# Optimization experiments

Hardware: AMD Instinct MI355X
Metric: run time of the kernel (lower is better)

The kernel has to match this reference:

```python
import jax, jax.numpy as jnp
import numpy as np

B = 131072     # batch of observations
OBS = 17       # HalfCheetah-v5 obs dim
ACT = 6        # HalfCheetah-v5 action dim
M = 16         # number of charts / experts
HID = 256      # encoder / value hidden width (hardcoded in module)
GHID = 128     # gate hidden width (hardcoded)
R = 24.0       # chart radius in whitened feature space
BETA = 1.0     # locality prior strength
NEG = -1e9     # masked-logit fill (finite to keep grads clean)
LOG_STD_MIN, LOG_STD_MAX = -20.0, 2.0


def setup_inputs() -> dict:
    key = jax.random.key(0)
    ks = jax.random.split(key, 12)
    def rn(i, shape, sc):
        return jax.random.normal(ks[i], shape, dtype=jnp.float32) * sc
    return {
        "obs": jax.random.normal(ks[0], (B, OBS), dtype=jnp.float32),
        # encoder MLP (only the two hidden tanh layers feed the feature 'feat')
        "W1": rn(1, (OBS, HID), 0.2), "b1": jnp.zeros((HID,), jnp.float32),
        "W2": rn(2, (HID, HID), 0.06), "b2": jnp.zeros((HID,), jnp.float32),
        # gate: Linear(256,128) -> tanh -> Linear(128,m)
        "Wg1": rn(3, (HID, GHID), 0.06), "bg1": jnp.zeros((GHID,), jnp.float32),
        "Wg2": rn(4, (GHID, M), 0.1), "bg2": jnp.zeros((M,), jnp.float32),
        # m local Gaussian heads: mu Linear(256, act), shared log_std param per head
        "muW": rn(5, (M, HID, ACT), 0.06), "mub": jnp.zeros((M, ACT), jnp.float32),
        "log_std": jnp.zeros((M, ACT), jnp.float32),
        # value head: 256 -> 256 -> 256 -> 1 with tanh
        "Wv1": rn(6, (HID, HID), 0.06), "bv1": jnp.zeros((HID,), jnp.float32),
        "Wv2": rn(7, (HID, HID), 0.06), "bv2": jnp.zeros((HID,), jnp.float32),
        "Wv3": rn(8, (HID, 1), 0.06), "bv3": jnp.zeros((1,), jnp.float32),
        # chart cover state (frozen params in the torch module)
        "centers": jax.random.normal(ks[9], (M, HID), dtype=jnp.float32),
        "stats_mean": jnp.zeros((HID,), jnp.float32),
        "stats_var": jnp.ones((HID,), jnp.float32),
    }


def reference(obs, W1, b1, W2, b2, Wg1, bg1, Wg2, bg2, muW, mub, log_std,
              Wv1, bv1, Wv2, bv2, Wv3, bv3, centers, stats_mean, stats_var):
    # shared encoder phi(o): two tanh layers -> feat [B, HID]
    feat = jnp.tanh(jnp.tanh(obs @ W1 + b1) @ W2 + b2)

    # whitened features and squared distances to chart centers (cdist via gram trick)
    zw = (feat - stats_mean) / jnp.sqrt(stats_var + 1e-6)          # [B, HID]
    d2 = jnp.maximum(
        jnp.sum(zw * zw, axis=-1, keepdims=True)
        + jnp.sum(centers * centers, axis=-1)
        - 2.0 * (zw @ centers.T), 0.0)                              # [B, M]
    dists = jnp.sqrt(d2)

    # gate logits + locality prior -beta * ||z - c_i||^2 / r^2
    logits = jnp.tanh(feat @ Wg1 + bg1) @ Wg2 + bg2 - BETA * d2 / (R * R)

    # masked softmax restricted to active charts; nearest chart always active
    active = dists <= R
    nearest = jax.nn.one_hot(jnp.argmin(dists, axis=1), M, dtype=bool)
    active = active | nearest
    g = jax.nn.softmax(jnp.where(active, logits, NEG), axis=1)      # [B, M]

    # local expert heads mu_i(z), then convex combination of mu and log_std
    mus = jnp.einsum('bd,mda->bma', feat, muW) + mub                # [B, M, ACT]
    mu_bar = jnp.einsum('bm,bma->ba', g, mus)                       # [B, ACT]
    s_bar = jnp.clip(g @ log_std, LOG_STD_MIN, LOG_STD_MAX)         # [B, ACT]

    # value head on shared features
    v = (jnp.tanh(jnp.tanh(feat @ Wv1 + bv1) @ Wv2 + bv2) @ Wv3 + bv3)[:, 0]
    return mu_bar, s_bar, v
```

## Files before the change

### kernel.cpp

```cpp
#include <hip/hip_runtime.h>
#include <hip/hip_bf16.h>

#define BDIM 256
#define TB 64
#define OBS_D 17
#define HID 256
#define GHID 128
#define NM 16
#define NACT 6

typedef __attribute__((ext_vector_type(8))) short short8;
typedef __attribute__((ext_vector_type(4))) float f32x4;

#define OFF_W1P    0u
#define OFF_W2P    16384u
#define OFF_WG1P   147456u
#define OFF_WG2P   212992u
#define OFF_CP     217088u
#define OFF_MUWP   225280u
#define OFF_WV1P   274432u
#define OFF_WV2P   405504u
#define OFF_CNORM  536576u
#define OFF_CCONST 536640u

__device__ __forceinline__ float tanh_fast(float x){
  float e = __expf(2.f * x);
  return fmaf(-2.f, __builtin_amdgcn_rcpf(e + 1.f), 1.f);
}
__device__ __forceinline__ short bf16b(float x){
  __hip_bfloat16 h = __float2bfloat16(x);
  return *reinterpret_cast<short*>(&h);
}

__global__ void prep_kernel(const float* __restrict__ W1, const float* __restrict__ W2,
    const float* __restrict__ Wg1, const float* __restrict__ Wg2,
    const float* __restrict__ muW, const float* __restrict__ Wv1, const float* __restrict__ Wv2,
    const float* __restrict__ centers, const float* __restrict__ smean, const float* __restrict__ svar,
    char* __restrict__ ws)
{
  __hip_bfloat16* w1p  = (__hip_bfloat16*)(ws + OFF_W1P);
  __hip_bfloat16* w2p  = (__hip_bfloat16*)(ws + OFF_W2P);
  __hip_bfloat16* wg1p = (__hip_bfloat16*)(ws + OFF_WG1P);
  __hip_bfloat16* wg2p = (__hip_bfloat16*)(ws + OFF_WG2P);
  __hip_bfloat16* cp   = (__hip_bfloat16*)(ws + OFF_CP);
  __hip_bfloat16* muwp = (__hip_bfloat16*)(ws + OFF_MUWP);
  __hip_bfloat16* wv1p = (__hip_bfloat16*)(ws + OFF_WV1P);
  __hip_bfloat16* wv2p = (__hip_bfloat16*)(ws + OFF_WV2P);
  float* cnorm  = (float*)(ws + OFF_CNORM);
  float* cconst = (float*)(ws + OFF_CCONST);

  int gid = blockIdx.x * blockDim.x + threadIdx.x;
  if (gid < NM){
    float s = 0.f; const float* c = centers + gid * HID;
    for (int k = 0; k < HID; ++k) s += c[k] * c[k];
    cnorm[gid] = s;
  } else if (gid < 2*NM){
    int m = gid - NM; float s = 0.f; const float* c = centers + m * HID;
    for (int k = 0; k < HID; ++k) s += smean[k] * rsqrtf(svar[k] + 1e-6f) * c[k];
    cconst[m] = s;
  }

  const int T0 = 8192, T1 = T0+65536, T2 = T1+32768, T3 = T2+2048,
            T4 = T3+4096, T5 = T4+24576, T6 = T5+65536, T7 = T6+65536;
  for (int i = gid; i < T7; i += gridDim.x * blockDim.x){
    float v; __hip_bfloat16* dst;
    if (i < T0){ int idx=i;    int kb8=idx/(256*8); int n=(idx/8)%256; int e=idx&7; int k=kb8*8+e;
      v = (k < OBS_D) ? W1[k*256+n] : 0.f; dst = &w1p[idx]; }
    else if (i < T1){ int idx=i-T0; int kb8=idx/(256*8); int n=(idx/8)%256; int e=idx&7; int k=kb8*8+e;
      v = W2[k*256+n]; dst = &w2p[idx]; }
    else if (i < T2){ int idx=i-T1; int kb8=idx/(128*8); int n=(idx/8)%128; int e=idx&7; int k=kb8*8+e;
      v = Wg1[k*128+n]; dst = &wg1p[idx]; }
    else if (i < T3){ int idx=i-T2; int kb8=idx/(16*8);  int n=(idx/8)%16;  int e=idx&7; int k=kb8*8+e;
      v = Wg2[k*16+n]; dst = &wg2p[idx]; }
    else if (i < T4){ int idx=i-T3; int kb8=idx/(16*8);  int m=(idx/8)%16;  int e=idx&7; int k=kb8*8+e;
      v = centers[m*HID+k] * rsqrtf(svar[k] + 1e-6f); dst = &cp[idx]; }
    else if (i < T5){ int idx=i-T4; int kb8=idx/(96*8);  int n=(idx/8)%96;  int e=idx&7; int k=kb8*8+e;
      int a = n >> 4, m = n & 15;
      v = muW[m*(HID*NACT) + k*NACT + a]; dst = &muwp[idx]; }
    else if (i < T6){ int idx=i-T5; int kb8=idx/(256*8); int n=(idx/8)%256; int e=idx&7; int k=kb8*8+e;
      v = Wv1[k*256+n]; dst = &wv1p[idx]; }
    else            { int idx=i-T6; int kb8=idx/(256*8); int n=(idx/8)%256; int e=idx&7; int k=kb8*8+e;
      v = Wv2[k*256+n]; dst = &wv2p[idx]; }
    *dst = __float2bfloat16(v);
  }
}

__global__ __launch_bounds__(BDIM, 2) void moe_kernel(
  const float* __restrict__ obs,
  const float* __restrict__ b1, const float* __restrict__ b2,
  const float* __restrict__ bg1, const float* __restrict__ bg2,
  const float* __restrict__ mub, const float* __restrict__ lstd,
  const float* __restrict__ bv1, const float* __restrict__ bv2,
  const float* __restrict__ Wv3, const float* __restrict__ bv3,
  const float* __restrict__ smean, const float* __restrict__ svar,
  const char* __restrict__ ws, float* __restrict__ out, int Btot)
{
  const short8* w1p  = (const short8*)(ws + OFF_W1P);
  const short8* w2p  = (const short8*)(ws + OFF_W2P);
  const short8* wg1p = (const short8*)(ws + OFF_WG1P);
  const short8* wg2p = (const short8*)(ws + OFF_WG2P);
  const short8* cp   = (const short8*)(ws + OFF_CP);
  const short8* muwp = (const short8*)(ws + OFF_MUWP);
  const short8* wv1p = (const short8*)(ws + OFF_WV1P);
  const short8* wv2p = (const short8*)(ws + OFF_WV2P);
  const float* cnorm  = (const float*)(ws + OFF_CNORM);
  const float* cconst = (const float*)(ws + OFF_CCONST);

  const int tid = threadIdx.x;
  const int w = tid >> 6, lane = tid & 63, l16 = lane & 15, lk = lane >> 4;
  const int rowg0 = blockIdx.x * TB;

  __shared__ __hip_bfloat16 feat_s[32*64*8];
  __shared__ __hip_bfloat16 sc_s[32*64*8];
  __shared__ float part_s[4][64];
  __shared__ float g_s[64*17];

  short8 aO[4];
  #pragma unroll
  for (int rt = 0; rt < 4; ++rt){
    const float* orow = obs + (size_t)(rowg0 + rt*16 + l16) * OBS_D;
    #pragma unroll
    for (int e = 0; e < 8; ++e){ int k = lk*8 + e; float v = (k < OBS_D) ? orow[k] : 0.f; aO[rt][e] = bf16b(v); }
  }
  #pragma unroll
  for (int ctl = 0; ctl < 4; ++ctl){
    const int ct = w*4 + ctl;
    short8 B = w1p[lk*256 + ct*16 + l16];
    const int col = ct*16 + l16; const float bb = b1[col];
    #pragma unroll
    for (int rt = 0; rt < 4; ++rt){
      f32x4 acc = {0.f,0.f,0.f,0.f};
      acc = __builtin_amdgcn_mfma_f32_16x16x32_bf16(aO[rt], B, acc, 0,0,0);
      #pragma unroll
      for (int r = 0; r < 4; ++r){
        int row = rt*16 + lk*4 + r;
        sc_s[((col>>3)*64 + row)*8 + (col&7)] = __float2bfloat16(tanh_fast(acc[r] + bb));
      }
    }
  }
  __syncthreads();

  {
    f32x4 acc[4][4];
    #pragma unroll
    for (int i = 0; i < 4; ++i)
      #pragma unroll
      for (int j = 0; j < 4; ++j) acc[i][j] = (f32x4){0.f,0.f,0.f,0.f};
    #pragma unroll
    for (int ck = 0; ck < 8; ++ck){
      short8 A[4];
      #pragma unroll
      for (int rt = 0; rt < 4; ++rt) A[rt] = *(const short8*)&sc_s[((ck*4+lk)*64 + rt*16 + l16)*8];
      #pragma unroll
      for (int ctl = 0; ctl < 4; ++ctl){
        short8 B = w2p[(ck*4+lk)*256 + (w*4+ctl)*16 + l16];
        #pragma unroll
        for (int rt = 0; rt < 4; ++rt)
          acc[ctl][rt] = __builtin_amdgcn_mfma_f32_16x16x32_bf16(A[rt], B, acc[ctl][rt], 0,0,0);
      }
    }
    float znp[16];
    #pragma unroll
    for (int i = 0; i < 16; ++i) znp[i] = 0.f;
    #pragma unroll
    for (int ctl = 0; ctl < 4; ++ctl){
      const int col = (w*4+ctl)*16 + l16;
      const float bb = b2[col], mn = smean[col], iv = rsqrtf(svar[col] + 1e-6f);
      #pragma unroll
      for (int rt = 0; rt < 4; ++rt){
        #pragma unroll
        for (int r = 0; r < 4; ++r){
          int row = rt*16 + lk*4 + r;
          __hip_bfloat16 fb = __float2bfloat16(tanh_fast(acc[ctl][rt][r] + bb));
          feat_s[((col>>3)*64 + row)*8 + (col&7)] = fb;
          float z = (__bfloat162float(fb) - mn) * iv;
          znp[rt*4+r] += z * z;
        }
      }
    }
    #pragma unroll
    for (int d = 1; d < 16; d <<= 1){
      #pragma unroll
      for (int i = 0; i < 16; ++i) znp[i] += __shfl_xor(znp[i], d, 64);
    }
    if (l16 == 0){
      #pragma unroll
      for (int i = 0; i < 16; ++i) part_s[w][(i>>2)*16 + lk*4 + (i&3)] = znp[i];
    }
  }
  __syncthreads();

  {
    f32x4 acc[2][4];
    #pragma unroll
    for (int i = 0; i < 2; ++i)
      #pragma unroll
      for (int j = 0; j < 4; ++j) acc[i][j] = (f32x4){0.f,0.f,0.f,0.f};
    #pragma unroll
    for (int ck = 0; ck < 8; ++ck){
      short8 A[4];
      #pragma unroll
      for (int rt = 0; rt < 4; ++rt) A[rt] = *(const short8*)&feat_s[((ck*4+lk)*64 + rt*16 + l16)*8];
      #pragma unroll
      for (int ctl = 0; ctl < 2; ++ctl){
        short8 B = wg1p[(ck*4+lk)*128 + (w*2+ctl)*16 + l16];
        #pragma unroll
        for (int rt = 0; rt < 4; ++rt)
          acc[ctl][rt] = __builtin_amdgcn_mfma_f32_16x16x32_bf16(A[rt], B, acc[ctl][rt], 0,0,0);
      }
    }
    #pragma unroll
    for (int ctl = 0; ctl < 2; ++ctl){
      const int col = (w*2+ctl)*16 + l16;
      const float bb = bg1[col];
      #pragma unroll
      for (int rt = 0; rt < 4; ++rt)
        #pragma unroll
        for (int r = 0; r < 4; ++r){
          int row = rt*16 + lk*4 + r;
          sc_s[((col>>3)*64 + row)*8 + (col&7)] = __float2bfloat16(tanh_fast(acc[ctl][rt][r] + bb));
        }
    }
  }
  __syncthreads();

  const int rw = w*16;
  short8 fF[8];
  #pragma unroll
  for (int ck = 0; ck < 8; ++ck) fF[ck] = *(const short8*)&feat_s[((ck*4+lk)*64 + rw + l16)*8];

  {
    f32x4 accL = {0.f,0.f,0.f,0.f};
    #pragma unroll
    for (int ks = 0; ks < 4; ++ks){
      short8 aT = *(const short8*)&sc_s[((ks*4+lk)*64 + rw + l16)*8];
      accL = __builtin_amdgcn_mfma_f32_16x16x32_bf16(aT, wg2p[(ks*4+lk)*16 + l16], accL, 0,0,0);
    }
    f32x4 accD = {0.f,0.f,0.f,0.f};
    #pragma unroll
    for (int ck = 0; ck < 8; ++ck)
      accD = __builtin_amdgcn_mfma_f32_16x16x32_bf16(fF[ck], cp[(ck*4+lk)*16 + l16], accD, 0,0,0);

    const float cn = cnorm[l16], cc = cconst[l16], bg2v = bg2[l16];
    float gw[4];
    #pragma unroll
    for (int r = 0; r < 4; ++r){
      int rowl = rw + lk*4 + r;
      float znr = part_s[0][rowl] + part_s[1][rowl] + part_s[2][rowl] + part_s[3][rowl];
      float dot = accD[r] - cc;
      float d2 = fmaxf(znr + cn - 2.f*dot, 0.f);
      float lg = accL[r] + bg2v - d2 * (1.f/(24.f*24.f));
      float mv = d2; int mi = l16;
      #pragma unroll
      for (int d = 1; d < 16; d <<= 1){
        float ov = __shfl_xor(mv, d, 64); int oi = __shfl_xor(mi, d, 64);
        if (ov < mv || (ov == mv && oi < mi)){ mv = ov; mi = oi; }
      }
      bool act = (d2 <= 576.f) || (mi == l16);
      lg = act ? lg : -1e9f;
      float mx = lg;
      #pragma unroll
      for (int d = 1; d < 16; d <<= 1) mx = fmaxf(mx, __shfl_xor(mx, d, 64));
      float ev = __expf(lg - mx);
      float sm = ev;
      #pragma unroll
      for (int d = 1; d < 16; d <<= 1) sm += __shfl_xor(sm, d, 64);
      gw[r] = ev * __builtin_amdgcn_rcpf(sm);
      g_s[rowl*17 + l16] = gw[r];
    }
    #pragma unroll
    for (int r = 0; r < 4; ++r){
      float sb[6];
      #pragma unroll
      for (int a = 0; a < 6; ++a) sb[a] = gw[r] * lstd[l16*6 + a];
      #pragma unroll
      for (int d = 1; d < 16; d <<= 1){
        #pragma unroll
        for (int a = 0; a < 6; ++a) sb[a] += __shfl_xor(sb[a], d, 64);
      }
      if (l16 == 0){
        int row = rowg0 + rw + lk*4 + r;
        #pragma unroll
        for (int a = 0; a < 6; ++a)
          out[(size_t)6*Btot + (size_t)row*6 + a] = fminf(fmaxf(sb[a], -20.f), 2.f);
      }
    }
  }
  __syncthreads();

  {
    const int na = (w < 2) ? 2 : 1;
    const int a0 = (w < 2) ? (w*2) : (w + 2);
    f32x4 acc[2][4];
    #pragma unroll
    for (int i = 0; i < 2; ++i)
      #pragma unroll
      for (int j = 0; j < 4; ++j) acc[i][j] = (f32x4){0.f,0.f,0.f,0.f};
    #pragma unroll
    for (int ck = 0; ck < 8; ++ck){
      short8 A[4];
      #pragma unroll
      for (int rt = 0; rt < 4; ++rt) A[rt] = *(const short8*)&feat_s[((ck*4+lk)*64 + rt*16 + l16)*8];
      #pragma unroll
      for (int al = 0; al < 2; ++al){
        if (al < na){
          short8 B = muwp[(ck*4+lk)*96 + (a0+al)*16 + l16];
          #pragma unroll
          for (int rt = 0; rt < 4; ++rt)
            acc[al][rt] = __builtin_amdgcn_mfma_f32_16x16x32_bf16(A[rt], B, acc[al][rt], 0,0,0);
        }
      }
    }
    #pragma unroll
    for (int al = 0; al < 2; ++al){
      if (al < na){
        const int a = a0 + al;
        const float mubv = mub[l16*6 + a];
        #pragma unroll
        for (int rt = 0; rt < 4; ++rt){
          #pragma unroll
          for (int r = 0; r < 4; ++r){
            int row = rt*16 + lk*4 + r;
            float m = (acc[al][rt][r] + mubv) * g_s[row*17 + l16];
            #pragma unroll
            for (int d = 1; d < 16; d <<= 1) m += __shfl_xor(m, d, 64);
            if (l16 == 0) out[(size_t)(rowg0 + row)*6 + a] = m;
          }
        }
      }
    }
  }

  {
    f32x4 acc[4][4];
    #pragma unroll
    for (int i = 0; i < 4; ++i)
      #pragma unroll
      for (int j = 0; j < 4; ++j) acc[i][j] = (f32x4){0.f,0.f,0.f,0.f};
    #pragma unroll
    for (int ck = 0; ck < 8; ++ck){
      short8 A[4];
      #pragma unroll
      for (int rt = 0; rt < 4; ++rt) A[rt] = *(const short8*)&feat_s[((ck*4+lk)*64 + rt*16 + l16)*8];
      #pragma unroll
      for (int ctl = 0; ctl < 4; ++ctl){
        short8 B = wv1p[(ck*4+lk)*256 + (w*4+ctl)*16 + l16];
        #pragma unroll
        for (int rt = 0; rt < 4; ++rt)
          acc[ctl][rt] = __builtin_amdgcn_mfma_f32_16x16x32_bf16(A[rt], B, acc[ctl][rt], 0,0,0);
      }
    }
    #pragma unroll
    for (int ctl = 0; ctl < 4; ++ctl){
      const int col = (w*4+ctl)*16 + l16;
      const float bb = bv1[col];
      #pragma unroll
      for (int rt = 0; rt < 4; ++rt)
        #pragma unroll
        for (int r = 0; r < 4; ++r){
          int row = rt*16 + lk*4 + r;
          sc_s[((col>>3)*64 + row)*8 + (col&7)] = __float2bfloat16(tanh_fast(acc[ctl][rt][r] + bb));
        }
    }
  }
  __syncthreads();

  {
    f32x4 acc[4][4];
    #pragma unroll
    for (int i = 0; i < 4; ++i)
      #pragma unroll
      for (int j = 0; j < 4; ++j) acc[i][j] = (f32x4){0.f,0.f,0.f,0.f};
    #pragma unroll
    for (int ck = 0; ck < 8; ++ck){
      short8 A[4];
      #pragma unroll
      for (int rt = 0; rt < 4; ++rt) A[rt] = *(const short8*)&sc_s[((ck*4+lk)*64 + rt*16 + l16)*8];
      #pragma unroll
      for (int ctl = 0; ctl < 4; ++ctl){
        short8 B = wv2p[(ck*4+lk)*256 + (w*4+ctl)*16 + l16];
        #pragma unroll
        for (int rt = 0; rt < 4; ++rt)
          acc[ctl][rt] = __builtin_amdgcn_mfma_f32_16x16x32_bf16(A[rt], B, acc[ctl][rt], 0,0,0);
      }
    }
    float vpp[16];
    #pragma unroll
    for (int i = 0; i < 16; ++i) vpp[i] = 0.f;
    #pragma unroll
    for (int ctl = 0; ctl < 4; ++ctl){
      const int col = (w*4+ctl)*16 + l16;
      const float bb = bv2[col], w3 = Wv3[col];
      #pragma unroll
      for (int rt = 0; rt < 4; ++rt)
        #pragma unroll
        for (int r = 0; r < 4; ++r)
          vpp[rt*4+r] += tanh_fast(acc[ctl][rt][r] + bb) * w3;
    }
    #pragma unroll
    for (int d = 1; d < 16; d <<= 1){
      #pragma unroll
      for (int i = 0; i < 16; ++i) vpp[i] += __shfl_xor(vpp[i], d, 64);
    }
    if (l16 == 0){
      #pragma unroll
      for (int i = 0; i < 16; ++i) part_s[w][(i>>2)*16 + lk*4 + (i&3)] = vpp[i];
    }
  }
  __syncthreads();
  if (lane < 16){
    int row = w*16 + lane;
    float v = part_s[0][row] + part_s[1][row] + part_s[2][row] + part_s[3][row] + bv3[0];
    out[(size_t)12*Btot + rowg0 + row] = v;
  }
}

extern "C" void kernel_launch(void* const* d_in, const int* in_sizes, int n_in,
                              void* d_out, int out_size, void* d_ws, size_t ws_size,
                              hipStream_t stream){
  const float* obs = (const float*)d_in[0];
  const float* W1  = (const float*)d_in[1];  const float* b1  = (const float*)d_in[2];
  const float* W2  = (const float*)d_in[3];  const float* b2  = (const float*)d_in[4];
  const float* Wg1 = (const float*)d_in[5];  const float* bg1 = (const float*)d_in[6];
  const float* Wg2 = (const float*)d_in[7];  const float* bg2 = (const float*)d_in[8];
  const float* muW = (const float*)d_in[9];  const float* mub = (const float*)d_in[10];
  const float* lstd= (const float*)d_in[11];
  const float* Wv1 = (const float*)d_in[12]; const float* bv1 = (const float*)d_in[13];
  const float* Wv2 = (const float*)d_in[14]; const float* bv2 = (const float*)d_in[15];
  const float* Wv3 = (const float*)d_in[16]; const float* bv3 = (const float*)d_in[17];
  const float* centers = (const float*)d_in[18];
  const float* smean   = (const float*)d_in[19];
  const float* svar    = (const float*)d_in[20];
  int Btot = in_sizes[0] / OBS_D;
  char* ws = (char*)d_ws;

  hipLaunchKernelGGL(prep_kernel, dim3(512), dim3(256), 0, stream,
      W1, W2, Wg1, Wg2, muW, Wv1, Wv2, centers, smean, svar, ws);
  hipLaunchKernelGGL(moe_kernel, dim3(Btot / TB), dim3(BDIM), 0, stream,
      obs, b1, b2, bg1, bg2, mub, lstd, bv1, bv2, Wv3, bv3, smean, svar,
      (const char*)ws, (float*)d_out, Btot);
}
```

Before: 187.4 us.

## Halve scratch LDS via split-K staging and fuse value layer with mu heads

The 256-wide scratch tile is cut to 128 columns, so the encoder layer 1 and value layer 1 outputs are produced in two halves and consumed by split-K accumulation into the next layer. The gate weights are stored in bf16, and the first half of value layer 1 is computed alongside the mu-head GEMM to reuse the loaded feature fragments. The chart-distance MFMA is folded into the gate layer-1 loop, and launch bounds move to 3 blocks per CU. Together these are meant to lower LDS and register pressure for higher occupancy, at the cost of extra barriers, recomputed feature loads, and possible register spills.

```diff
diff --git a/kernel.cpp b/kernel.cpp
--- a/kernel.cpp
+++ b/kernel.cpp
@@ -85,7 +85,7 @@
   }
 }
 
-__global__ __launch_bounds__(BDIM, 2) void moe_kernel(
+__global__ __launch_bounds__(BDIM, 3) void moe_kernel(
   const float* __restrict__ obs,
   const float* __restrict__ b1, const float* __restrict__ b2,
   const float* __restrict__ bg1, const float* __restrict__ bg2,
@@ -109,11 +109,12 @@
   const int tid = threadIdx.x;
   const int w = tid >> 6, lane = tid & 63, l16 = lane & 15, lk = lane >> 4;
   const int rowg0 = blockIdx.x * TB;
+  const int rw = w*16;
 
   __shared__ __hip_bfloat16 feat_s[32*64*8];
-  __shared__ __hip_bfloat16 sc_s[32*64*8];
+  __shared__ __hip_bfloat16 sc_s[16*64*8];
   __shared__ float part_s[4][64];
-  __shared__ float g_s[64*17];
+  __shared__ __hip_bfloat16 g_s[64*18];
 
   short8 aO[4];
   #pragma unroll
@@ -122,9 +123,10 @@
     #pragma unroll
     for (int e = 0; e < 8; ++e){ int k = lk*8 + e; float v = (k < OBS_D) ? orow[k] : 0.f; aO[rt][e] = bf16b(v); }
   }
-  #pragma unroll
-  for (int ctl = 0; ctl < 4; ++ctl){
-    const int ct = w*4 + ctl;
+
+  #pragma unroll
+  for (int ctl = 0; ctl < 2; ++ctl){
+    const int ct = w*2 + ctl;
     short8 B = w1p[lk*256 + ct*16 + l16];
     const int col = ct*16 + l16; const float bb = b1[col];
     #pragma unroll
@@ -140,73 +142,109 @@
   }
   __syncthreads();
 
+  f32x4 acc2[4][4];
+  #pragma unroll
+  for (int i = 0; i < 4; ++i)
+    #pragma unroll
+    for (int j = 0; j < 4; ++j) acc2[i][j] = (f32x4){0.f,0.f,0.f,0.f};
+  #pragma unroll
+  for (int ck = 0; ck < 4; ++ck){
+    short8 A[4];
+    #pragma unroll
+    for (int rt = 0; rt < 4; ++rt) A[rt] = *(const short8*)&sc_s[((ck*4+lk)*64 + rt*16 + l16)*8];
+    #pragma unroll
+    for (int ctl = 0; ctl < 4; ++ctl){
+      short8 B = w2p[(ck*4+lk)*256 + (w*4+ctl)*16 + l16];
+      #pragma unroll
+      for (int rt = 0; rt < 4; ++rt)
+        acc2[ctl][rt] = __builtin_amdgcn_mfma_f32_16x16x32_bf16(A[rt], B, acc2[ctl][rt], 0,0,0);
+    }
+  }
+  __syncthreads();
+
+  #pragma unroll
+  for (int ctl = 0; ctl < 2; ++ctl){
+    const int ct = 8 + w*2 + ctl;
+    short8 B = w1p[lk*256 + ct*16 + l16];
+    const int col = ct*16 + l16; const float bb = b1[col];
+    #pragma unroll
+    for (int rt = 0; rt < 4; ++rt){
+      f32x4 acc = {0.f,0.f,0.f,0.f};
+      acc = __builtin_amdgcn_mfma_f32_16x16x32_bf16(aO[rt], B, acc, 0,0,0);
+      #pragma unroll
+      for (int r = 0; r < 4; ++r){
+        int row = rt*16 + lk*4 + r;
+        sc_s[((((col-128)>>3))*64 + row)*8 + (col&7)] = __float2bfloat16(tanh_fast(acc[r] + bb));
+      }
+    }
+  }
+  __syncthreads();
+
+  #pragma unroll
+  for (int ck = 4; ck < 8; ++ck){
+    short8 A[4];
+    #pragma unroll
+    for (int rt = 0; rt < 4; ++rt) A[rt] = *(const short8*)&sc_s[((ck*4+lk-16)*64 + rt*16 + l16)*8];
+    #pragma unroll
+    for (int ctl = 0; ctl < 4; ++ctl){
+      short8 B = w2p[(ck*4+lk)*256 + (w*4+ctl)*16 + l16];
+      #pragma unroll
+      for (int rt = 0; rt < 4; ++rt)
+        acc2[ctl][rt] = __builtin_amdgcn_mfma_f32_16x16x32_bf16(A[rt], B, acc2[ctl][rt], 0,0,0);
+    }
+  }
   {
-    f32x4 acc[4][4];
-    #pragma unroll
-    for (int i = 0; i < 4; ++i)
-      #pragma unroll
-      for (int j = 0; j < 4; ++j) acc[i][j] = (f32x4){0.f,0.f,0.f,0.f};
+    float znp[16];
+    #pragma unroll
+    for (int i = 0; i < 16; ++i) znp[i] = 0.f;
+    #pragma unroll
+    for (int ctl = 0; ctl < 4; ++ctl){
+      const int col = (w*4+ctl)*16 + l16;
+      const float bb = b2[col], mn = smean[col], iv = rsqrtf(svar[col] + 1e-6f);
+      #pragma unroll
+      for (int rt = 0; rt < 4; ++rt){
+        #pragma unroll
+        for (int r = 0; r < 4; ++r){
+          int row = rt*16 + lk*4 + r;
+          float tf = tanh_fast(acc2[ctl][rt][r] + bb);
+          feat_s[((col>>3)*64 + row)*8 + (col&7)] = __float2bfloat16(tf);
+          float z = (tf - mn) * iv;
+          znp[rt*4+r] += z * z;
+        }
+      }
+    }
+    #pragma unroll
+    for (int d = 1; d < 16; d <<= 1){
+      #pragma unroll
+      for (int i = 0; i < 16; ++i) znp[i] += __shfl_xor(znp[i], d, 64);
+    }
+    if (l16 == 0){
+      #pragma unroll
+      for (int i = 0; i < 16; ++i) part_s[w][(i>>2)*16 + lk*4 + (i&3)] = znp[i];
+    }
+  }
+  __syncthreads();
+
+  f32x4 accD = {0.f,0.f,0.f,0.f};
+  {
+    f32x4 acc3[2][4];
+    #pragma unroll
+    for (int i = 0; i < 2; ++i)
+      #pragma unroll
+      for (int j = 0; j < 4; ++j) acc3[i][j] = (f32x4){0.f,0.f,0.f,0.f};
     #pragma unroll
     for (int ck = 0; ck < 8; ++ck){
       short8 A[4];
       #pragma unroll
-      for (int rt = 0; rt < 4; ++rt) A[rt] = *(const short8*)&sc_s[((ck*4+lk)*64 + rt*16 + l16)*8];
-      #pragma unroll
-      for (int ctl = 0; ctl < 4; ++ctl){
-        short8 B = w2p[(ck*4+lk)*256 + (w*4+ctl)*16 + l16];
-        #pragma unroll
-        for (int rt = 0; rt < 4; ++rt)
-          acc[ctl][rt] = __builtin_amdgcn_mfma_f32_16x16x32_bf16(A[rt], B, acc[ctl][rt], 0,0,0);
-      }
-    }
-    float znp[16];
-    #pragma unroll
-    for (int i = 0; i < 16; ++i) znp[i] = 0.f;
-    #pragma unroll
-    for (int ctl = 0; ctl < 4; ++ctl){
-      const int col = (w*4+ctl)*16 + l16;
-      const float bb = b2[col], mn = smean[col], iv = rsqrtf(svar[col] + 1e-6f);
-      #pragma unroll
-      for (int rt = 0; rt < 4; ++rt){
-        #pragma unroll
-        for (int r = 0; r < 4; ++r){
-          int row = rt*16 + lk*4 + r;
-          __hip_bfloat16 fb = __float2bfloat16(tanh_fast(acc[ctl][rt][r] + bb));
-          feat_s[((col>>3)*64 + row)*8 + (col&7)] = fb;
-          float z = (__bfloat162float(fb) - mn) * iv;
-          znp[rt*4+r] += z * z;
-        }
-      }
-    }
-    #pragma unroll
-    for (int d = 1; d < 16; d <<= 1){
-      #pragma unroll
-      for (int i = 0; i < 16; ++i) znp[i] += __shfl_xor(znp[i], d, 64);
-    }
-    if (l16 == 0){
-      #pragma unroll
-      for (int i = 0; i < 16; ++i) part_s[w][(i>>2)*16 + lk*4 + (i&3)] = znp[i];
-    }
-  }
-  __syncthreads();
-
-  {
-    f32x4 acc[2][4];
-    #pragma unroll
-    for (int i = 0; i < 2; ++i)
-      #pragma unroll
-      for (int j = 0; j < 4; ++j) acc[i][j] = (f32x4){0.f,0.f,0.f,0.f};
-    #pragma unroll
-    for (int ck = 0; ck < 8; ++ck){
-      short8 A[4];
-      #pragma unroll
       for (int rt = 0; rt < 4; ++rt) A[rt] = *(const short8*)&feat_s[((ck*4+lk)*64 + rt*16 + l16)*8];
+      short8 Af = *(const short8*)&feat_s[((ck*4+lk)*64 + rw + l16)*8];
+      accD = __builtin_amdgcn_mfma_f32_16x16x32_bf16(Af, cp[(ck*4+lk)*16 + l16], accD, 0,0,0);
       #pragma unroll
       for (int ctl = 0; ctl < 2; ++ctl){
         short8 B = wg1p[(ck*4+lk)*128 + (w*2+ctl)*16 + l16];
         #pragma unroll
         for (int rt = 0; rt < 4; ++rt)
-          acc[ctl][rt] = __builtin_amdgcn_mfma_f32_16x16x32_bf16(A[rt], B, acc[ctl][rt], 0,0,0);
+          acc3[ctl][rt] = __builtin_amdgcn_mfma_f32_16x16x32_bf16(A[rt], B, acc3[ctl][rt], 0,0,0);
       }
     }
     #pragma unroll
@@ -218,16 +256,11 @@
         #pragma unroll
         for (int r = 0; r < 4; ++r){
           int row = rt*16 + lk*4 + r;
-          sc_s[((col>>3)*64 + row)*8 + (col&7)] = __float2bfloat16(tanh_fast(acc[ctl][rt][r] + bb));
+          sc_s[((col>>3)*64 + row)*8 + (col&7)] = __float2bfloat16(tanh_fast(acc3[ctl][rt][r] + bb));
         }
     }
   }
   __syncthreads();
-
-  const int rw = w*16;
-  short8 fF[8];
-  #pragma unroll
-  for (int ck = 0; ck < 8; ++ck) fF[ck] = *(const short8*)&feat_s[((ck*4+lk)*64 + rw + l16)*8];
 
   {
     f32x4 accL = {0.f,0.f,0.f,0.f};
@@ -236,11 +269,6 @@
       short8 aT = *(const short8*)&sc_s[((ks*4+lk)*64 + rw + l16)*8];
       accL = __builtin_amdgcn_mfma_f32_16x16x32_bf16(aT, wg2p[(ks*4+lk)*16 + l16], accL, 0,0,0);
     }
-    f32x4 accD = {0.f,0.f,0.f,0.f};
-    #pragma unroll
-    for (int ck = 0; ck < 8; ++ck)
-      accD = __builtin_amdgcn_mfma_f32_16x16x32_bf16(fF[ck], cp[(ck*4+lk)*16 + l16], accD, 0,0,0);
-
     const float cn = cnorm[l16], cc = cconst[l16], bg2v = bg2[l16];
     float gw[4];
     #pragma unroll
@@ -266,7 +294,7 @@
       #pragma unroll
       for (int d = 1; d < 16; d <<= 1) sm += __shfl_xor(sm, d, 64);
       gw[r] = ev * __builtin_amdgcn_rcpf(sm);
-      g_s[rowl*17 + l16] = gw[r];
+      g_s[rowl*18 + l16] = __float2bfloat16(gw[r]);
     }
     #pragma unroll
     for (int r = 0; r < 4; ++r){
@@ -291,11 +319,11 @@
   {
     const int na = (w < 2) ? 2 : 1;
     const int a0 = (w < 2) ? (w*2) : (w + 2);
-    f32x4 acc[2][4];
+    f32x4 accM[2][4], acc7[2][4];
     #pragma unroll
     for (int i = 0; i < 2; ++i)
       #pragma unroll
-      for (int j = 0; j < 4; ++j) acc[i][j] = (f32x4){0.f,0.f,0.f,0.f};
+      for (int j = 0; j < 4; ++j){ accM[i][j] = (f32x4){0.f,0.f,0.f,0.f}; acc7[i][j] = (f32x4){0.f,0.f,0.f,0.f}; }
     #pragma unroll
     for (int ck = 0; ck < 8; ++ck){
       short8 A[4];
@@ -304,12 +332,31 @@
       #pragma unroll
       for (int al = 0; al < 2; ++al){
         if (al < na){
-          short8 B = muwp[(ck*4+lk)*96 + (a0+al)*16 + l16];
+          short8 Bm = muwp[(ck*4+lk)*96 + (a0+al)*16 + l16];
           #pragma unroll
           for (int rt = 0; rt < 4; ++rt)
-            acc[al][rt] = __builtin_amdgcn_mfma_f32_16x16x32_bf16(A[rt], B, acc[al][rt], 0,0,0);
+            accM[al][rt] = __builtin_amdgcn_mfma_f32_16x16x32_bf16(A[rt], Bm, accM[al][rt], 0,0,0);
         }
       }
+      #pragma unroll
+      for (int ctl = 0; ctl < 2; ++ctl){
+        short8 Bv = wv1p[(ck*4+lk)*256 + (w*2+ctl)*16 + l16];
+        #pragma unroll
+        for (int rt = 0; rt < 4; ++rt)
+          acc7[ctl][rt] = __builtin_amdgcn_mfma_f32_16x16x32_bf16(A[rt], Bv, acc7[ctl][rt], 0,0,0);
+      }
+    }
+    #pragma unroll
+    for (int ctl = 0; ctl < 2; ++ctl){
+      const int col = (w*2+ctl)*16 + l16;
+      const float bb = bv1[col];
+      #pragma unroll
+      for (int rt = 0; rt < 4; ++rt)
+        #pragma unroll
+        for (int r = 0; r < 4; ++r){
+          int row = rt*16 + lk*4 + r;
+          sc_s[((col>>3)*64 + row)*8 + (col&7)] = __float2bfloat16(tanh_fast(acc7[ctl][rt][r] + bb));
+        }
     }
     #pragma unroll
     for (int al = 0; al < 2; ++al){
@@ -321,7 +368,7 @@
           #pragma unroll
           for (int r = 0; r < 4; ++r){
             int row = rt*16 + lk*4 + r;
-            float m = (acc[al][rt][r] + mubv) * g_s[row*17 + l16];
+            float m = (accM[al][rt][r] + mubv) * __bfloat162float(g_s[row*18 + l16]);
             #pragma unroll
             for (int d = 1; d < 16; d <<= 1) m += __shfl_xor(m, d, 64);
             if (l16 == 0) out[(size_t)(rowg0 + row)*6 + a] = m;
@@ -330,60 +377,69 @@
       }
     }
   }
-
+  __syncthreads();
+
+  f32x4 acc8[4][4];
+  #pragma unroll
+  for (int i = 0; i < 4; ++i)
+    #pragma unroll
+    for (int j = 0; j < 4; ++j) acc8[i][j] = (f32x4){0.f,0.f,0.f,0.f};
+  #pragma unroll
+  for (int ck = 0; ck < 4; ++ck){
+    short8 A[4];
+    #pragma unroll
+    for (int rt = 0; rt < 4; ++rt) A[rt] = *(const short8*)&sc_s[((ck*4+lk)*64 + rt*16 + l16)*8];
+    #pragma unroll
+    for (int ctl = 0; ctl < 4; ++ctl){
+      short8 B = wv2p[(ck*4+lk)*256 + (w*4+ctl)*16 + l16];
+      #pragma unroll
+      for (int rt = 0; rt < 4; ++rt)
+        acc8[ctl][rt] = __builtin_amdgcn_mfma_f32_16x16x32_bf16(A[rt], B, acc8[ctl][rt], 0,0,0);
+    }
+  }
+  __syncthreads();
+
+  #pragma unroll
+  for (int ctl = 0; ctl < 2; ++ctl){
+    const int ct = 8 + w*2 + ctl;
+    f32x4 accv[4];
+    #pragma unroll
+    for (int rt = 0; rt < 4; ++rt) accv[rt] = (f32x4){0.f,0.f,0.f,0.f};
+    #pragma unroll
+    for (int ck = 0; ck < 8; ++ck){
+      short8 B = wv1p[(ck*4+lk)*256 + ct*16 + l16];
+      #pragma unroll
+      for (int rt = 0; rt < 4; ++rt){
+        short8 A = *(const short8*)&feat_s[((ck*4+lk)*64 + rt*16 + l16)*8];
+        accv[rt] = __builtin_amdgcn_mfma_f32_16x16x32_bf16(A, B, accv[rt], 0,0,0);
+      }
+    }
+    const int col = ct*16 + l16;
+    const float bb = bv1[col];
+    #pragma unroll
+    for (int rt = 0; rt < 4; ++rt)
+      #pragma unroll
+      for (int r = 0; r < 4; ++r){
+        int row = rt*16 + lk*4 + r;
+        sc_s[((((col-128)>>3))*64 + row)*8 + (col&7)] = __float2bfloat16(tanh_fast(accv[rt][r] + bb));
+      }
+  }
+  __syncthreads();
+
+  #pragma unroll
+  for (int ck = 4; ck < 8; ++ck){
+    short8 A[4];
+    #pragma unroll
+    for (int rt = 0; rt < 4; ++rt) A[rt] = *(const short8*)&sc_s[((ck*4+lk-16)*64 + rt*16 + l16)*8];
+    #pragma unroll
+    for (int ctl = 0; ctl < 4; ++ctl){
+      short8 B = wv2p[(ck*4+lk)*256 + (w*4+ctl)*16 + l16];
+      #pragma unroll
+      for (int rt = 0; rt < 4; ++rt)
+        acc8[ctl][rt] = __builtin_amdgcn_mfma_f32_16x16x32_bf16(A[rt], B, acc8[ctl][rt], 0,0,0);
+    }
+  }
   {
-    f32x4 acc[4][4];
-    #pragma unroll
-    for (int i = 0; i < 4; ++i)
-      #pragma unroll
-      for (int j = 0; j < 4; ++j) acc[i][j] = (f32x4){0.f,0.f,0.f,0.f};
-    #pragma unroll
-    for (int ck = 0; ck < 8; ++ck){
-      short8 A[4];
-      #pragma unroll
-      for (int rt = 0; rt < 4; ++rt) A[rt] = *(const short8*)&feat_s[((ck*4+lk)*64 + rt*16 + l16)*8];
-      #pragma unroll
-      for (int ctl = 0; ctl < 4; ++ctl){
-        short8 B = wv1p[(ck*4+lk)*256 + (w*4+ctl)*16 + l16];
-        #pragma unroll
-        for (int rt = 0; rt < 4; ++rt)
-          acc[ctl][rt] = __builtin_amdgcn_mfma_f32_16x16x32_bf16(A[rt], B, acc[ctl][rt], 0,0,0);
-      }
-    }
-    #pragma unroll
-    for (int ctl = 0; ctl < 4; ++ctl){
-      const int col = (w*4+ctl)*16 + l16;
-      const float bb = bv1[col];
-      #pragma unroll
-      for (int rt = 0; rt < 4; ++rt)
-        #pragma unroll
-        for (int r = 0; r < 4; ++r){
-          int row = rt*16 + lk*4 + r;
-          sc_s[((col>>3)*64 + row)*8 + (col&7)] = __float2bfloat16(tanh_fast(acc[ctl][rt][r] + bb));
-        }
-    }
-  }
-  __syncthreads();
-
-  {
-    f32x4 acc[4][4];
-    #pragma unroll
-    for (int i = 0; i < 4; ++i)
-      #pragma unroll
-      for (int j = 0; j < 4; ++j) acc[i][j] = (f32x4){0.f,0.f,0.f,0.f};
-    #pragma unroll
-    for (int ck = 0; ck < 8; ++ck){
-      short8 A[4];
-      #pragma unroll
-      for (int rt = 0; rt < 4; ++rt) A[rt] = *(const short8*)&sc_s[((ck*4+lk)*64 + rt*16 + l16)*8];
-      #pragma unroll
-      for (int ctl = 0; ctl < 4; ++ctl){
-        short8 B = wv2p[(ck*4+lk)*256 + (w*4+ctl)*16 + l16];
-        #pragma unroll
-        for (int rt = 0; rt < 4; ++rt)
-          acc[ctl][rt] = __builtin_amdgcn_mfma_f32_16x16x32_bf16(A[rt], B, acc[ctl][rt], 0,0,0);
-      }
-    }
     float vpp[16];
     #pragma unroll
     for (int i = 0; i < 16; ++i) vpp[i] = 0.f;
@@ -395,7 +451,7 @@
       for (int rt = 0; rt < 4; ++rt)
         #pragma unroll
         for (int r = 0; r < 4; ++r)
-          vpp[rt*4+r] += tanh_fast(acc[ctl][rt][r] + bb) * w3;
+          vpp[rt*4+r] += tanh_fast(acc8[ctl][rt][r] + bb) * w3;
     }
     #pragma unroll
     for (int d = 1; d < 16; d <<= 1){
```

New measurement: 203.1 us. 1.08x slower.

## Double block to 8 waves and overlap gate, mixture and value stages across waves

Applied to the files above, without the earlier changes.

The fused MoE kernel now runs 8 waves per 64-row tile instead of 4, so each wave owns half as many output column tiles in every GEMM stage. The stages are rescheduled so that independent work runs on different waves at the same time. Waves 0-3 do the gate logits and softmax while waves 4-7 start the value layer-1 columns. Then waves 0-3 finish value layer 1 while waves 4-7 compute the expert mu mixture, which removes one barrier-separated phase. The center-distance MFMA is folded into the gate layer-1 loop, and z-norms now use the fp32 tanh value rather than the bf16-rounded one. The cost is higher register pressure from launch bounds (512,4) and more divergent branches per wave.

```diff
diff --git a/kernel.cpp b/kernel.cpp
--- a/kernel.cpp
+++ b/kernel.cpp
@@ -1,7 +1,7 @@
 #include <hip/hip_runtime.h>
 #include <hip/hip_bf16.h>
 
-#define BDIM 256
+#define BDIM 512
 #define TB 64
 #define OBS_D 17
 #define HID 256
@@ -85,7 +85,7 @@
   }
 }
 
-__global__ __launch_bounds__(BDIM, 2) void moe_kernel(
+__global__ __launch_bounds__(BDIM, 4) void moe_kernel(
   const float* __restrict__ obs,
   const float* __restrict__ b1, const float* __restrict__ b2,
   const float* __restrict__ bg1, const float* __restrict__ bg2,
@@ -112,7 +112,7 @@
 
   __shared__ __hip_bfloat16 feat_s[32*64*8];
   __shared__ __hip_bfloat16 sc_s[32*64*8];
-  __shared__ float part_s[4][64];
+  __shared__ float part_s[8][64];
   __shared__ float g_s[64*17];
 
   short8 aO[4];
@@ -122,9 +122,10 @@
     #pragma unroll
     for (int e = 0; e < 8; ++e){ int k = lk*8 + e; float v = (k < OBS_D) ? orow[k] : 0.f; aO[rt][e] = bf16b(v); }
   }
+
   #pragma unroll
-  for (int ctl = 0; ctl < 4; ++ctl){
-    const int ct = w*4 + ctl;
+  for (int ctl = 0; ctl < 2; ++ctl){
+    const int ct = w*2 + ctl;
     short8 B = w1p[lk*256 + ct*16 + l16];
     const int col = ct*16 + l16; const float bb = b1[col];
     #pragma unroll
@@ -141,39 +142,39 @@
   __syncthreads();
 
   {
-    f32x4 acc[4][4];
-    #pragma unroll
-    for (int i = 0; i < 4; ++i)
-      #pragma unroll
-      for (int j = 0; j < 4; ++j) acc[i][j] = (f32x4){0.f,0.f,0.f,0.f};
+    f32x4 acc2[2][4];
+    #pragma unroll
+    for (int i = 0; i < 2; ++i)
+      #pragma unroll
+      for (int j = 0; j < 4; ++j) acc2[i][j] = (f32x4){0.f,0.f,0.f,0.f};
     #pragma unroll
     for (int ck = 0; ck < 8; ++ck){
       short8 A[4];
       #pragma unroll
       for (int rt = 0; rt < 4; ++rt) A[rt] = *(const short8*)&sc_s[((ck*4+lk)*64 + rt*16 + l16)*8];
       #pragma unroll
-      for (int ctl = 0; ctl < 4; ++ctl){
-        short8 B = w2p[(ck*4+lk)*256 + (w*4+ctl)*16 + l16];
+      for (int ctl = 0; ctl < 2; ++ctl){
+        short8 B = w2p[(ck*4+lk)*256 + (w*2+ctl)*16 + l16];
         #pragma unroll
         for (int rt = 0; rt < 4; ++rt)
-          acc[ctl][rt] = __builtin_amdgcn_mfma_f32_16x16x32_bf16(A[rt], B, acc[ctl][rt], 0,0,0);
+          acc2[ctl][rt] = __builtin_amdgcn_mfma_f32_16x16x32_bf16(A[rt], B, acc2[ctl][rt], 0,0,0);
       }
     }
     float znp[16];
     #pragma unroll
     for (int i = 0; i < 16; ++i) znp[i] = 0.f;
     #pragma unroll
-    for (int ctl = 0; ctl < 4; ++ctl){
-      const int col = (w*4+ctl)*16 + l16;
+    for (int ctl = 0; ctl < 2; ++ctl){
+      const int col = (w*2+ctl)*16 + l16;
       const float bb = b2[col], mn = smean[col], iv = rsqrtf(svar[col] + 1e-6f);
       #pragma unroll
       for (int rt = 0; rt < 4; ++rt){
         #pragma unroll
         for (int r = 0; r < 4; ++r){
           int row = rt*16 + lk*4 + r;
-          __hip_bfloat16 fb = __float2bfloat16(tanh_fast(acc[ctl][rt][r] + bb));
-          feat_s[((col>>3)*64 + row)*8 + (col&7)] = fb;
-          float z = (__bfloat162float(fb) - mn) * iv;
+          float tf = tanh_fast(acc2[ctl][rt][r] + bb);
+          feat_s[((col>>3)*64 + row)*8 + (col&7)] = __float2bfloat16(tf);
+          float z = (tf - mn) * iv;
           znp[rt*4+r] += z * z;
         }
       }
@@ -190,66 +191,54 @@
   }
   __syncthreads();
 
+  f32x4 accD = {0.f,0.f,0.f,0.f};
   {
-    f32x4 acc[2][4];
-    #pragma unroll
-    for (int i = 0; i < 2; ++i)
-      #pragma unroll
-      for (int j = 0; j < 4; ++j) acc[i][j] = (f32x4){0.f,0.f,0.f,0.f};
+    f32x4 acc3[4];
+    #pragma unroll
+    for (int j = 0; j < 4; ++j) acc3[j] = (f32x4){0.f,0.f,0.f,0.f};
     #pragma unroll
     for (int ck = 0; ck < 8; ++ck){
       short8 A[4];
       #pragma unroll
       for (int rt = 0; rt < 4; ++rt) A[rt] = *(const short8*)&feat_s[((ck*4+lk)*64 + rt*16 + l16)*8];
-      #pragma unroll
-      for (int ctl = 0; ctl < 2; ++ctl){
-        short8 B = wg1p[(ck*4+lk)*128 + (w*2+ctl)*16 + l16];
-        #pragma unroll
-        for (int rt = 0; rt < 4; ++rt)
-          acc[ctl][rt] = __builtin_amdgcn_mfma_f32_16x16x32_bf16(A[rt], B, acc[ctl][rt], 0,0,0);
-      }
-    }
-    #pragma unroll
-    for (int ctl = 0; ctl < 2; ++ctl){
-      const int col = (w*2+ctl)*16 + l16;
-      const float bb = bg1[col];
+      if (w < 4)
+        accD = __builtin_amdgcn_mfma_f32_16x16x32_bf16(A[w], cp[(ck*4+lk)*16 + l16], accD, 0,0,0);
+      short8 B = wg1p[(ck*4+lk)*128 + w*16 + l16];
       #pragma unroll
       for (int rt = 0; rt < 4; ++rt)
-        #pragma unroll
-        for (int r = 0; r < 4; ++r){
-          int row = rt*16 + lk*4 + r;
-          sc_s[((col>>3)*64 + row)*8 + (col&7)] = __float2bfloat16(tanh_fast(acc[ctl][rt][r] + bb));
-        }
-    }
-  }
-  __syncthreads();
-
-  const int rw = w*16;
-  short8 fF[8];
-  #pragma unroll
-  for (int ck = 0; ck < 8; ++ck) fF[ck] = *(const short8*)&feat_s[((ck*4+lk)*64 + rw + l16)*8];
-
-  {
+        acc3[rt] = __builtin_amdgcn_mfma_f32_16x16x32_bf16(A[rt], B, acc3[rt], 0,0,0);
+    }
+    const int col = w*16 + l16;
+    const float bb = bg1[col];
+    #pragma unroll
+    for (int rt = 0; rt < 4; ++rt)
+      #pragma unroll
+      for (int r = 0; r < 4; ++r){
+        int row = rt*16 + lk*4 + r;
+        sc_s[((col>>3)*64 + row)*8 + (col&7)] = __float2bfloat16(tanh_fast(acc3[rt][r] + bb));
+      }
+  }
+  __syncthreads();
+
+  if (w < 4){
+    const int rw = w*16;
     f32x4 accL = {0.f,0.f,0.f,0.f};
     #pragma unroll
     for (int ks = 0; ks < 4; ++ks){
       short8 aT = *(const short8*)&sc_s[((ks*4+lk)*64 + rw + l16)*8];
       accL = __builtin_amdgcn_mfma_f32_16x16x32_bf16(aT, wg2p[(ks*4+lk)*16 + l16], accL, 0,0,0);
     }
-    f32x4 accD = {0.f,0.f,0.f,0.f};
-    #pragma unroll
-    for (int ck = 0; ck < 8; ++ck)
-      accD = __builtin_amdgcn_mfma_f32_16x16x32_bf16(fF[ck], cp[(ck*4+lk)*16 + l16], accD, 0,0,0);
-
     const float cn = cnorm[l16], cc = cconst[l16], bg2v = bg2[l16];
     float gw[4];
     #pragma unroll
     for (int r = 0; r < 4; ++r){
       int rowl = rw + lk*4 + r;
-      float znr = part_s[0][rowl] + part_s[1][rowl] + part_s[2][rowl] + part_s[3][rowl];
+      float znr = 0.f;
+      #pragma unroll
+      for (int i = 0; i < 8; ++i) znr += part_s[i][rowl];
       float dot = accD[r] - cc;
       float d2 = fmaxf(znr + cn - 2.f*dot, 0.f);
-      float lg = accL[r] + bg2v - d2 * (1.f/(24.f*24.f));
+      float lg = accL[r] + bg2v - d2 * (1.f/576.f);
       float mv = d2; int mi = l16;
       #pragma unroll
       for (int d = 1; d < 16; d <<= 1){
@@ -285,17 +274,79 @@
           out[(size_t)6*Btot + (size_t)row*6 + a] = fminf(fmaxf(sb[a], -20.f), 2.f);
       }
     }
-  }
-  __syncthreads();
-
-  {
-    const int na = (w < 2) ? 2 : 1;
-    const int a0 = (w < 2) ? (w*2) : (w + 2);
-    f32x4 acc[2][4];
+  } else {
+    f32x4 acc7[2][4];
     #pragma unroll
     for (int i = 0; i < 2; ++i)
       #pragma unroll
-      for (int j = 0; j < 4; ++j) acc[i][j] = (f32x4){0.f,0.f,0.f,0.f};
+      for (int j = 0; j < 4; ++j) acc7[i][j] = (f32x4){0.f,0.f,0.f,0.f};
+    #pragma unroll
+    for (int ck = 0; ck < 8; ++ck){
+      short8 A[4];
+      #pragma unroll
+      for (int rt = 0; rt < 4; ++rt) A[rt] = *(const short8*)&feat_s[((ck*4+lk)*64 + rt*16 + l16)*8];
+      #pragma unroll
+      for (int ctl = 0; ctl < 2; ++ctl){
+        short8 B = wv1p[(ck*4+lk)*256 + (8 + (w-4)*2 + ctl)*16 + l16];
+        #pragma unroll
+        for (int rt = 0; rt < 4; ++rt)
+          acc7[ctl][rt] = __builtin_amdgcn_mfma_f32_16x16x32_bf16(A[rt], B, acc7[ctl][rt], 0,0,0);
+      }
+    }
+    #pragma unroll
+    for (int ctl = 0; ctl < 2; ++ctl){
+      const int col = (8 + (w-4)*2 + ctl)*16 + l16;
+      const float bb = bv1[col];
+      #pragma unroll
+      for (int rt = 0; rt < 4; ++rt)
+        #pragma unroll
+        for (int r = 0; r < 4; ++r){
+          int row = rt*16 + lk*4 + r;
+          sc_s[((col>>3)*64 + row)*8 + (col&7)] = __float2bfloat16(tanh_fast(acc7[ctl][rt][r] + bb));
+        }
+    }
+  }
+  __syncthreads();
+
+  if (w < 4){
+    f32x4 acc7[2][4];
+    #pragma unroll
+    for (int i = 0; i < 2; ++i)
+      #pragma unroll
+      for (int j = 0; j < 4; ++j) acc7[i][j] = (f32x4){0.f,0.f,0.f,0.f};
+    #pragma unroll
+    for (int ck = 0; ck < 8; ++ck){
+      short8 A[4];
+      #pragma unroll
+      for (int rt = 0; rt < 4; ++rt) A[rt] = *(const short8*)&feat_s[((ck*4+lk)*64 + rt*16 + l16)*8];
+      #pragma unroll
+      for (int ctl = 0; ctl < 2; ++ctl){
+        short8 B = wv1p[(ck*4+lk)*256 + (w*2 + ctl)*16 + l16];
+        #pragma unroll
+        for (int rt = 0; rt < 4; ++rt)
+          acc7[ctl][rt] = __builtin_amdgcn_mfma_f32_16x16x32_bf16(A[rt], B, acc7[ctl][rt], 0,0,0);
+      }
+    }
+    #pragma unroll
+    for (int ctl = 0; ctl < 2; ++ctl){
+      const int col = (w*2 + ctl)*16 + l16;
+      const float bb = bv1[col];
+      #pragma unroll
+      for (int rt = 0; rt < 4; ++rt)
+        #pragma unroll
+        for (int r = 0; r < 4; ++r){
+          int row = rt*16 + lk*4 + r;
+          sc_s[((col>>3)*64 + row)*8 + (col&7)] = __float2bfloat16(tanh_fast(acc7[ctl][rt][r] + bb));
+        }
+    }
+  } else {
+    const int na = (w < 6) ? 2 : 1;
+    const int a0 = (w < 6) ? (w-4)*2 : (w-2);
+    f32x4 accM[2][4];
+    #pragma unroll
+    for (int i = 0; i < 2; ++i)
+      #pragma unroll
+      for (int j = 0; j < 4; ++j) accM[i][j] = (f32x4){0.f,0.f,0.f,0.f};
     #pragma unroll
     for (int ck = 0; ck < 8; ++ck){
       short8 A[4];
@@ -307,7 +358,7 @@
           short8 B = muwp[(ck*4+lk)*96 + (a0+al)*16 + l16];
           #pragma unroll
           for (int rt = 0; rt < 4; ++rt)
-            acc[al][rt] = __builtin_amdgcn_mfma_f32_16x16x32_bf16(A[rt], B, acc[al][rt], 0,0,0);
+            accM[al][rt] = __builtin_amdgcn_mfma_f32_16x16x32_bf16(A[rt], B, accM[al][rt], 0,0,0);
         }
       }
     }
@@ -321,7 +372,7 @@
           #pragma unroll
           for (int r = 0; r < 4; ++r){
             int row = rt*16 + lk*4 + r;
-            float m = (acc[al][rt][r] + mubv) * g_s[row*17 + l16];
+            float m = (accM[al][rt][r] + mubv) * g_s[row*17 + l16];
             #pragma unroll
             for (int d = 1; d < 16; d <<= 1) m += __shfl_xor(m, d, 64);
             if (l16 == 0) out[(size_t)(rowg0 + row)*6 + a] = m;
@@ -330,72 +381,39 @@
       }
     }
   }
+  __syncthreads();
 
   {
-    f32x4 acc[4][4];
-    #pragma unroll
-    for (int i = 0; i < 4; ++i)
-      #pragma unroll
-      for (int j = 0; j < 4; ++j) acc[i][j] = (f32x4){0.f,0.f,0.f,0.f};
-    #pragma unroll
-    for (int ck = 0; ck < 8; ++ck){
-      short8 A[4];
-      #pragma unroll
-      for (int rt = 0; rt < 4; ++rt) A[rt] = *(const short8*)&feat_s[((ck*4+lk)*64 + rt*16 + l16)*8];
-      #pragma unroll
-      for (int ctl = 0; ctl < 4; ++ctl){
-        short8 B = wv1p[(ck*4+lk)*256 + (w*4+ctl)*16 + l16];
+    f32x4 acc8[2][4];
+    #pragma unroll
+    for (int i = 0; i < 2; ++i)
+      #pragma unroll
+      for (int j = 0; j < 4; ++j) acc8[i][j] = (f32x4){0.f,0.f,0.f,0.f};
+    #pragma unroll
+    for (int ck = 0; ck < 8; ++ck){
+      short8 A[4];
+      #pragma unroll
+      for (int rt = 0; rt < 4; ++rt) A[rt] = *(const short8*)&sc_s[((ck*4+lk)*64 + rt*16 + l16)*8];
+      #pragma unroll
+      for (int ctl = 0; ctl < 2; ++ctl){
+        short8 B = wv2p[(ck*4+lk)*256 + (w*2+ctl)*16 + l16];
         #pragma unroll
         for (int rt = 0; rt < 4; ++rt)
-          acc[ctl][rt] = __builtin_amdgcn_mfma_f32_16x16x32_bf16(A[rt], B, acc[ctl][rt], 0,0,0);
-      }
-    }
-    #pragma unroll
-    for (int ctl = 0; ctl < 4; ++ctl){
-      const int col = (w*4+ctl)*16 + l16;
-      const float bb = bv1[col];
+          acc8[ctl][rt] = __builtin_amdgcn_mfma_f32_16x16x32_bf16(A[rt], B, acc8[ctl][rt], 0,0,0);
+      }
+    }
+    float vpp[16];
+    #pragma unroll
+    for (int i = 0; i < 16; ++i) vpp[i] = 0.f;
+    #pragma unroll
+    for (int ctl = 0; ctl < 2; ++ctl){
+      const int col = (w*2+ctl)*16 + l16;
+      const float bb = bv2[col], w3 = Wv3[col];
       #pragma unroll
       for (int rt = 0; rt < 4; ++rt)
         #pragma unroll
-        for (int r = 0; r < 4; ++r){
-          int row = rt*16 + lk*4 + r;
-          sc_s[((col>>3)*64 + row)*8 + (col&7)] = __float2bfloat16(tanh_fast(acc[ctl][rt][r] + bb));
-        }
-    }
-  }
-  __syncthreads();
-
-  {
-    f32x4 acc[4][4];
-    #pragma unroll
-    for (int i = 0; i < 4; ++i)
-      #pragma unroll
-      for (int j = 0; j < 4; ++j) acc[i][j] = (f32x4){0.f,0.f,0.f,0.f};
-    #pragma unroll
-    for (int ck = 0; ck < 8; ++ck){
-      short8 A[4];
-      #pragma unroll
-      for (int rt = 0; rt < 4; ++rt) A[rt] = *(const short8*)&sc_s[((ck*4+lk)*64 + rt*16 + l16)*8];
-      #pragma unroll
-      for (int ctl = 0; ctl < 4; ++ctl){
-        short8 B = wv2p[(ck*4+lk)*256 + (w*4+ctl)*16 + l16];
-        #pragma unroll
-        for (int rt = 0; rt < 4; ++rt)
-          acc[ctl][rt] = __builtin_amdgcn_mfma_f32_16x16x32_bf16(A[rt], B, acc[ctl][rt], 0,0,0);
-      }
-    }
-    float vpp[16];
-    #pragma unroll
-    for (int i = 0; i < 16; ++i) vpp[i] = 0.f;
-    #pragma unroll
-    for (int ctl = 0; ctl < 4; ++ctl){
-      const int col = (w*4+ctl)*16 + l16;
-      const float bb = bv2[col], w3 = Wv3[col];
-      #pragma unroll
-      for (int rt = 0; rt < 4; ++rt)
-        #pragma unroll
         for (int r = 0; r < 4; ++r)
-          vpp[rt*4+r] += tanh_fast(acc[ctl][rt][r] + bb) * w3;
+          vpp[rt*4+r] += tanh_fast(acc8[ctl][rt][r] + bb) * w3;
     }
     #pragma unroll
     for (int d = 1; d < 16; d <<= 1){
@@ -408,10 +426,11 @@
     }
   }
   __syncthreads();
-  if (lane < 16){
-    int row = w*16 + lane;
-    float v = part_s[0][row] + part_s[1][row] + part_s[2][row] + part_s[3][row] + bv3[0];
-    out[(size_t)12*Btot + rowg0 + row] = v;
+  if (tid < 64){
+    float v = bv3[0];
+    #pragma unroll
+    for (int i = 0; i < 8; ++i) v += part_s[i][tid];
+    out[(size_t)12*Btot + rowg0 + tid] = v;
   }
 }
 
```

Measured after the change: 209.2 us. +11.7%, slower.
